# Kernel optimization log

Hardware: AMD Instinct MI355X
Metric: run time of the kernel (lower is better)

The kernel has to match this reference:

```python
import jax, jax.numpy as jnp
import numpy as np

MAX_DEG = 3
DEG_DIMS = [1, 3, 5, 7]          # degree_to_dim(d) = 2d+1
SUM_DIM = 16                     # sum of DEG_DIMS
FREQ_SUM = 44                    # sum over (d_in,d_out) of 2*min(d_in,d_out)+1
C = 32                           # channels per degree (in == out, FULL fusion)
EDGE_DIM = 2                     # fiber_edge[0] + 1
MID = 32                         # RadialProfile mid_dim
E = 4096
N = 1024


def setup_inputs() -> dict:
    key = jax.random.key(0)
    ks = jax.random.split(key, 16)
    inp = {}
    for d, dim in enumerate(DEG_DIMS):
        inp[f"node_feats_{d}"] = jax.random.normal(ks[d], (N, C, dim), jnp.float32)
    inp["edge_feats_0"] = jax.random.normal(ks[4], (E, EDGE_DIM, 1), jnp.float32)
    inp["basis"] = jax.random.normal(ks[5], (E, SUM_DIM, FREQ_SUM, SUM_DIM), jnp.float32)
    inp["src"] = jax.random.randint(ks[6], (E,), 0, N, dtype=jnp.int32)
    inp["dst"] = jax.random.randint(ks[7], (E,), 0, N, dtype=jnp.int32)
    # RadialProfile params: Linear(2,32) -> ReLU -> Linear(32,32) -> ReLU -> Linear(32, 44*32*32, bias=False)
    inp["w1"] = jax.random.normal(ks[8], (EDGE_DIM, MID), jnp.float32) / np.sqrt(EDGE_DIM)
    inp["b1"] = jnp.zeros((MID,), jnp.float32)
    inp["w2"] = jax.random.normal(ks[9], (MID, MID), jnp.float32) / np.sqrt(MID)
    inp["b2"] = jnp.zeros((MID,), jnp.float32)
    inp["w3"] = jax.random.normal(ks[10], (MID, FREQ_SUM * C * C), jnp.float32) / np.sqrt(MID)
    # self-interaction kernels per output degree
    for d in range(MAX_DEG + 1):
        inp[f"kernel_self_{d}"] = jax.random.normal(ks[11 + d], (C, C), jnp.float32) / np.sqrt(C)
    return inp


def _conv_se3(node_feats, edge_feats_0, basis, src, dst,
              w1, b1, w2, b2, w3, kernels_self):
    e = edge_feats_0.shape[0]
    # invariant edge feats: [E, edge_dim]
    inv = edge_feats_0[..., 0]
    # gather source node features and fuse along representation dim: [E, C, 16]
    feats = jnp.concatenate([nf[src] for nf in node_feats], axis=-1)
    # RadialProfile MLP -> radial weights [E, C_out, C_in * FREQ_SUM]
    h = jax.nn.relu(inv @ w1 + b1)
    h = jax.nn.relu(h @ w2 + b2)
    radial_weights = (h @ w3).reshape(e, C, C * FREQ_SUM)
    # VersatileConvSE3 fused path:
    # tmp = (features @ basis_view).view(E, C*FREQ_SUM, SUM_DIM)
    basis_view = basis.reshape(e, SUM_DIM, FREQ_SUM * SUM_DIM)
    tmp = jnp.einsum('eci,eix->ecx', feats, basis_view).reshape(e, C * FREQ_SUM, SUM_DIM)
    out_fused = jnp.einsum('eok,eks->eos', radial_weights, tmp)  # [E, C, 16]
    # unfuse by degree, add self-interaction at dst, pool (copy_e_sum) to nodes
    outs = []
    off = 0
    for d, dim in enumerate(DEG_DIMS):
        o = out_fused[..., off:off + dim]
        o = o + jnp.einsum('oc,ecd->eod', kernels_self[d], node_feats[d][dst])
        outs.append(jax.ops.segment_sum(o, dst, num_segments=N))
        off += dim
    # return fused node output [N, C, 16] (concat of degrees 0..3)
    return jnp.concatenate(outs, axis=-1)


def reference(node_feats_0, node_feats_1, node_feats_2, node_feats_3,
              edge_feats_0, basis, src, dst,
              w1, b1, w2, b2, w3,
              kernel_self_0, kernel_self_1, kernel_self_2, kernel_self_3):
    return _conv_se3([node_feats_0, node_feats_1, node_feats_2, node_feats_3],
                     edge_feats_0, basis, src, dst,
                     w1, b1, w2, b2, w3,
                     [kernel_self_0, kernel_self_1, kernel_self_2, kernel_self_3])
```

## Files before the change

### kernel.cpp

```cpp
#include <hip/hip_runtime.h>
#include <hip/hip_bf16.h>

#define NN 1024
#define EE 4096
#define CC 32
#define SD 16
#define FQ 44
#define MIDC 32
#define EB 16
#define NFQ 4
#define FPB 11

typedef short s16x4 __attribute__((ext_vector_type(4)));
typedef short s16x8 __attribute__((ext_vector_type(8)));
typedef float fx4 __attribute__((ext_vector_type(4)));

__device__ __forceinline__ unsigned short f2b(float x) {
    __hip_bfloat16 b = __float2bfloat16(x);
    return *reinterpret_cast<unsigned short*>(&b);
}

__device__ __forceinline__ s16x4 pack4(float a, float b, float c, float d) {
    s16x4 r;
    r[0] = (short)f2b(a); r[1] = (short)f2b(b);
    r[2] = (short)f2b(c); r[3] = (short)f2b(d);
    return r;
}

__device__ __forceinline__ fx4 mfma16(s16x4 a, s16x4 b, fx4 c) {
#if defined(__HIP_DEVICE_COMPILE__)
#if __has_builtin(__builtin_amdgcn_mfma_f32_16x16x16_bf16)
    return __builtin_amdgcn_mfma_f32_16x16x16_bf16(a, b, c, 0, 0, 0);
#else
    return __builtin_amdgcn_mfma_f32_16x16x16bf16_1k(a, b, c, 0, 0, 0);
#endif
#else
    return c;
#endif
}

#define CBAR() asm volatile("s_waitcnt lgkmcnt(0)\n\ts_barrier" ::: "memory")
#define MEMFENCE() asm volatile("" ::: "memory")

__global__ __launch_bounds__(256) void k_w3t2(const float* __restrict__ w3,
                                              unsigned short* __restrict__ w3t2) {
    int tid = blockIdx.x * 256 + threadIdx.x;
    int m = tid & 31;
    int o = (tid >> 5) & 31;
    int c = tid >> 10;
    const float* rp = &w3[(size_t)m * 45056 + o * 1408 + c * 44];
    float v[44];
#pragma unroll
    for (int q = 0; q < 11; q++) {
        float4 t4 = *(const float4*)(rp + q * 4);
        v[q * 4 + 0] = t4.x; v[q * 4 + 1] = t4.y;
        v[q * 4 + 2] = t4.z; v[q * 4 + 3] = t4.w;
    }
#pragma unroll
    for (int f = 0; f < FQ; f++) {
        w3t2[(((size_t)f * CC + o) * CC + c) * CC + m] = f2b(v[f]);
    }
}

__global__ __launch_bounds__(256) void k_h(const float* __restrict__ ef,
                                           const float* __restrict__ w1,
                                           const float* __restrict__ b1,
                                           const float* __restrict__ w2,
                                           const float* __restrict__ b2,
                                           const int* __restrict__ dst,
                                           unsigned short* __restrict__ h2,
                                           int* __restrict__ deg) {
    int e = blockIdx.x * 256 + threadIdx.x;
    if (e >= EE) return;
    float i0 = ef[e * 2 + 0], i1 = ef[e * 2 + 1];
    float h1[MIDC];
#pragma unroll
    for (int j = 0; j < MIDC; j++) {
        float v = i0 * w1[j] + i1 * w1[MIDC + j] + b1[j];
        h1[j] = v > 0.f ? v : 0.f;
    }
    for (int j = 0; j < MIDC; j++) {
        float v = b2[j];
#pragma unroll
        for (int m = 0; m < MIDC; m++) v += h1[m] * w2[m * MIDC + j];
        v = v > 0.f ? v : 0.f;
        h2[e * MIDC + j] = f2b(v);
    }
    atomicAdd(&deg[dst[e]], 1);
}

__global__ __launch_bounds__(512, 4) void k_main(
    const float* __restrict__ nf0, const float* __restrict__ nf1,
    const float* __restrict__ nf2, const float* __restrict__ nf3,
    const float* __restrict__ basis, const int* __restrict__ src,
    const int* __restrict__ dst, const unsigned short* __restrict__ h2,
    const unsigned short* __restrict__ w3t2, float* __restrict__ out) {
    __shared__ __align__(16) unsigned short rad_lds[EB * CC * CC];

    int t = threadIdx.x;
    int wv = t >> 6;
    int l = t & 63;
    int l15 = l & 15;
    int kg = l >> 4;
    int fq = blockIdx.x >> 8;
    int eg = blockIdx.x & 255;
    int eb = eg * EB;
    int f0 = fq * FPB;

    s16x8 h2frag = *(const s16x8*)(h2 + ((size_t)(eb + l15) * MIDC + (kg << 3)));

    s16x4 fa[2][2];
#pragma unroll
    for (int ei = 0; ei < 2; ei++) {
        int sn = src[eb + (wv << 1) + ei];
#pragma unroll
        for (int ch = 0; ch < 2; ch++) {
            int c = (ch << 4) + l15;
            s16x4 v;
#pragma unroll
            for (int j = 0; j < 4; j++) {
                int i = (kg << 2) + j;
                float x;
                if (i < 1) x = nf0[sn * CC + c];
                else if (i < 4) x = nf1[(sn * CC + c) * 3 + (i - 1)];
                else if (i < 9) x = nf2[(sn * CC + c) * 5 + (i - 4)];
                else x = nf3[(sn * CC + c) * 7 + (i - 9)];
                v[j] = (short)f2b(x);
            }
            fa[ei][ch] = v;
        }
    }

    int radw[8];
#pragma unroll
    for (int j = 0; j < 8; j++) {
        int o = (wv << 2) + (j >> 1), ch = j & 1;
        int b = (l15 << 11) | (o << 6) | (ch << 5) | (kg << 3);
        radw[j] = b ^ (((l15 ^ o) & 15) << 3);
    }
    int rada[2][2][2];
#pragma unroll
    for (int ei = 0; ei < 2; ei++) {
        int e = (wv << 1) + ei;
#pragma unroll
        for (int oh = 0; oh < 2; oh++) {
            int o = (oh << 4) + l15;
#pragma unroll
            for (int ch = 0; ch < 2; ch++) {
                int b = (e << 11) | (o << 6) | (ch << 5) | (kg << 3);
                rada[ei][oh][ch] = b ^ (((e ^ o) & 15) << 3);
            }
        }
    }

    fx4 acc[2][2];
#pragma unroll
    for (int q = 0; q < 4; q++) acc[q >> 1][q & 1] = (fx4){0.f, 0.f, 0.f, 0.f};
    fx4 zz = (fx4){0.f, 0.f, 0.f, 0.f};

    s16x8 w[8];
    float pfA[2][4], pfB[2][4];

#define LOAD_W(F)                                                                       \
    {                                                                                   \
        _Pragma("unroll") for (int j = 0; j < 8; j++) {                                 \
            int o_ = (wv << 2) + (j >> 1), ch_ = j & 1;                                 \
            w[j] = *(const s16x8*)(w3t2 +                                               \
                ((((size_t)(F) * CC + o_) * CC + (ch_ << 4) + l15) * CC + (kg << 3)));  \
        }                                                                               \
        MEMFENCE();                                                                     \
    }
#define LOAD_PF(F, SLOT)                                                                \
    {                                                                                   \
        _Pragma("unroll") for (int ei_ = 0; ei_ < 2; ei_++) {                           \
            const float* bp = basis +                                                   \
                (((size_t)(eb + (wv << 1) + ei_) * SD + (kg << 2)) * FQ + (F)) * SD +   \
                l15;                                                                    \
            _Pragma("unroll") for (int j = 0; j < 4; j++)                               \
                SLOT[ei_][j] = bp[(size_t)j * (FQ * SD)];                               \
        }                                                                               \
        MEMFENCE();                                                                     \
    }

    LOAD_PF(f0, pfA);
    LOAD_W(f0);
    LOAD_PF(f0 + 1, pfB);

#pragma unroll
    for (int fi = 0; fi < FPB; fi++) {
        int f = f0 + fi;
#pragma unroll
        for (int j = 0; j < 8; j++) {
            fx4 cf = __builtin_amdgcn_mfma_f32_16x16x32_bf16(w[j], h2frag, zz, 0, 0, 0);
            *(s16x4*)((char*)rad_lds + radw[j]) = pack4(cf[0], cf[1], cf[2], cf[3]);
        }
        if (fi + 1 < FPB) LOAD_W(f + 1);

        s16x4 bbf[2];
        if ((fi & 1) == 0) {
            bbf[0] = pack4(pfA[0][0], pfA[0][1], pfA[0][2], pfA[0][3]);
            bbf[1] = pack4(pfA[1][0], pfA[1][1], pfA[1][2], pfA[1][3]);
            if (fi + 2 < FPB) { LOAD_PF(f + 2, pfA); }
        } else {
            bbf[0] = pack4(pfB[0][0], pfB[0][1], pfB[0][2], pfB[0][3]);
            bbf[1] = pack4(pfB[1][0], pfB[1][1], pfB[1][2], pfB[1][3]);
            if (fi + 2 < FPB) { LOAD_PF(f + 2, pfB); }
        }
        CBAR();

#pragma unroll
        for (int ei = 0; ei < 2; ei++) {
#pragma unroll
            for (int ch = 0; ch < 2; ch++) {
                fx4 u = mfma16(fa[ei][ch], bbf[ei], zz);
                s16x4 ub = pack4(u[0], u[1], u[2], u[3]);
#pragma unroll
                for (int oh = 0; oh < 2; oh++) {
                    s16x4 ra = *(const s16x4*)((char*)rad_lds + rada[ei][oh][ch]);
                    acc[ei][oh] = mfma16(ra, ub, acc[ei][oh]);
                }
            }
        }
        if (fi + 1 < FPB) CBAR();
    }

#pragma unroll
    for (int ei = 0; ei < 2; ei++) {
        int e = (wv << 1) + ei;
        int d = dst[eb + e];
        float* op = &out[(size_t)d * (CC * SD)];
#pragma unroll
        for (int oh = 0; oh < 2; oh++) {
#pragma unroll
            for (int r = 0; r < 4; r++) {
                int o = (oh << 4) + (kg << 2) + r;
                atomicAdd(&op[o * SD + l15], acc[ei][oh][r]);
            }
        }
    }
}

__global__ __launch_bounds__(256) void k_self(
    const float* __restrict__ nf0, const float* __restrict__ nf1,
    const float* __restrict__ nf2, const float* __restrict__ nf3,
    const float* __restrict__ ks0, const float* __restrict__ ks1,
    const float* __restrict__ ks2, const float* __restrict__ ks3,
    const int* __restrict__ deg, float* __restrict__ out) {
    int idx = blockIdx.x * 256 + threadIdx.x;
    if (idx >= NN * CC * SD) return;
    int n = idx >> 9;
    int rem = idx & 511;
    int o = rem >> 4;
    int s = rem & 15;
    const float* nf;
    const float* ks;
    int dim, off;
    if (s < 1) { nf = nf0; ks = ks0; dim = 1; off = 0; }
    else if (s < 4) { nf = nf1; ks = ks1; dim = 3; off = 1; }
    else if (s < 9) { nf = nf2; ks = ks2; dim = 5; off = 4; }
    else { nf = nf3; ks = ks3; dim = 7; off = 9; }
    int j = s - off;
    float acc = 0.f;
#pragma unroll
    for (int c = 0; c < CC; c++) acc += ks[o * CC + c] * nf[(n * CC + c) * dim + j];
    out[idx] += (float)deg[n] * acc;
}

extern "C" void kernel_launch(void* const* d_in, const int* in_sizes, int n_in,
                              void* d_out, int out_size, void* d_ws, size_t ws_size,
                              hipStream_t stream) {
    const float* nf0 = (const float*)d_in[0];
    const float* nf1 = (const float*)d_in[1];
    const float* nf2 = (const float*)d_in[2];
    const float* nf3 = (const float*)d_in[3];
    const float* ef = (const float*)d_in[4];
    const float* basis = (const float*)d_in[5];
    const int* src = (const int*)d_in[6];
    const int* dst = (const int*)d_in[7];
    const float* w1 = (const float*)d_in[8];
    const float* b1 = (const float*)d_in[9];
    const float* w2 = (const float*)d_in[10];
    const float* b2 = (const float*)d_in[11];
    const float* w3 = (const float*)d_in[12];
    const float* ks0 = (const float*)d_in[13];
    const float* ks1 = (const float*)d_in[14];
    const float* ks2 = (const float*)d_in[15];
    const float* ks3 = (const float*)d_in[16];
    float* out = (float*)d_out;

    unsigned short* h2 = (unsigned short*)d_ws;
    int* deg = (int*)((char*)d_ws + EE * MIDC * 2);
    unsigned short* w3t2 = (unsigned short*)((char*)d_ws + EE * MIDC * 2 + 4096);

    (void)hipMemsetAsync(d_out, 0, (size_t)out_size * sizeof(float), stream);
    (void)hipMemsetAsync(deg, 0, NN * sizeof(int), stream);

    k_w3t2<<<128, 256, 0, stream>>>(w3, w3t2);
    k_h<<<EE / 256, 256, 0, stream>>>(ef, w1, b1, w2, b2, dst, h2, deg);
    k_main<<<(EE / EB) * NFQ, 512, 0, stream>>>(nf0, nf1, nf2, nf3, basis, src, dst,
                                                h2, w3t2, out);
    k_self<<<(NN * CC * SD) / 256, 256, 0, stream>>>(nf0, nf1, nf2, nf3, ks0, ks1,
                                                     ks2, ks3, deg, out);
}
```

Baseline: 126.6 us.

## Stage basis slice into LDS with coalesced float4 loads before frequency loop

```diff
diff --git a/kernel.cpp b/kernel.cpp
--- a/kernel.cpp
+++ b/kernel.cpp
@@ -10,6 +10,8 @@
 #define EB 16
 #define NFQ 4
 #define FPB 11
+#define FSTR 264
+#define ESTR (FPB * FSTR)
 
 typedef short s16x4 __attribute__((ext_vector_type(4)));
 typedef short s16x8 __attribute__((ext_vector_type(8)));
@@ -89,19 +91,19 @@
     atomicAdd(&deg[dst[e]], 1);
 }
 
-__global__ __launch_bounds__(512, 4) void k_main(
+__global__ __launch_bounds__(512, 2) void k_main(
     const float* __restrict__ nf0, const float* __restrict__ nf1,
     const float* __restrict__ nf2, const float* __restrict__ nf3,
     const float* __restrict__ basis, const int* __restrict__ src,
     const int* __restrict__ dst, const unsigned short* __restrict__ h2,
     const unsigned short* __restrict__ w3t2, float* __restrict__ out) {
     __shared__ __align__(16) unsigned short rad_lds[EB * CC * CC];
+    __shared__ __align__(16) unsigned short basT[EB * ESTR];
 
     int t = threadIdx.x;
     int wv = t >> 6;
-    int l = t & 63;
-    int l15 = l & 15;
-    int kg = l >> 4;
+    int l15 = t & 15;
+    int kg = (t >> 4) & 3;
     int fq = blockIdx.x >> 8;
     int eg = blockIdx.x & 255;
     int eb = eg * EB;
@@ -131,6 +133,21 @@
         }
     }
 
+#pragma unroll
+    for (int k = 0; k < 22; k++) {
+        int fi4 = k * 512 + t;
+        int g = fi4 / 44;
+        int r = fi4 - g * 44;
+        int e = g >> 4, i = g & 15;
+        const float4* sp = (const float4*)basis +
+                           (((size_t)(eb + e) * SD + i) * 176 + fq * 44 + r);
+        float4 v = *sp;
+        int perm = ((i & 3) << 2) | (i >> 2);
+        int f1 = r >> 2, s0 = (r & 3) << 2;
+        *(s16x4*)(&basT[e * ESTR + f1 * FSTR + perm * 16 + s0]) =
+            pack4(v.x, v.y, v.z, v.w);
+    }
+
     int radw[8];
 #pragma unroll
     for (int j = 0; j < 8; j++) {
@@ -159,8 +176,6 @@
     fx4 zz = (fx4){0.f, 0.f, 0.f, 0.f};
 
     s16x8 w[8];
-    float pfA[2][4], pfB[2][4];
-
 #define LOAD_W(F)                                                                       \
     {                                                                                   \
         _Pragma("unroll") for (int j = 0; j < 8; j++) {                                 \
@@ -170,44 +185,35 @@
         }                                                                               \
         MEMFENCE();                                                                     \
     }
-#define LOAD_PF(F, SLOT)                                                                \
-    {                                                                                   \
-        _Pragma("unroll") for (int ei_ = 0; ei_ < 2; ei_++) {                           \
-            const float* bp = basis +                                                   \
-                (((size_t)(eb + (wv << 1) + ei_) * SD + (kg << 2)) * FQ + (F)) * SD +   \
-                l15;                                                                    \
-            _Pragma("unroll") for (int j = 0; j < 4; j++)                               \
-                SLOT[ei_][j] = bp[(size_t)j * (FQ * SD)];                               \
-        }                                                                               \
-        MEMFENCE();                                                                     \
-    }
-
-    LOAD_PF(f0, pfA);
+
     LOAD_W(f0);
-    LOAD_PF(f0 + 1, pfB);
+    __syncthreads();
 
 #pragma unroll
     for (int fi = 0; fi < FPB; fi++) {
         int f = f0 + fi;
+        __builtin_amdgcn_s_setprio(1);
 #pragma unroll
         for (int j = 0; j < 8; j++) {
             fx4 cf = __builtin_amdgcn_mfma_f32_16x16x32_bf16(w[j], h2frag, zz, 0, 0, 0);
             *(s16x4*)((char*)rad_lds + radw[j]) = pack4(cf[0], cf[1], cf[2], cf[3]);
         }
+        __builtin_amdgcn_s_setprio(0);
         if (fi + 1 < FPB) LOAD_W(f + 1);
 
         s16x4 bbf[2];
-        if ((fi & 1) == 0) {
-            bbf[0] = pack4(pfA[0][0], pfA[0][1], pfA[0][2], pfA[0][3]);
-            bbf[1] = pack4(pfA[1][0], pfA[1][1], pfA[1][2], pfA[1][3]);
-            if (fi + 2 < FPB) { LOAD_PF(f + 2, pfA); }
-        } else {
-            bbf[0] = pack4(pfB[0][0], pfB[0][1], pfB[0][2], pfB[0][3]);
-            bbf[1] = pack4(pfB[1][0], pfB[1][1], pfB[1][2], pfB[1][3]);
-            if (fi + 2 < FPB) { LOAD_PF(f + 2, pfB); }
+#pragma unroll
+        for (int ei = 0; ei < 2; ei++) {
+            const unsigned short* bp =
+                &basT[((wv << 1) + ei) * ESTR + fi * FSTR + (kg << 4) + l15];
+            s16x4 v;
+#pragma unroll
+            for (int j = 0; j < 4; j++) v[j] = (short)bp[j << 6];
+            bbf[ei] = v;
         }
         CBAR();
 
+        __builtin_amdgcn_s_setprio(1);
 #pragma unroll
         for (int ei = 0; ei < 2; ei++) {
 #pragma unroll
@@ -221,6 +227,7 @@
                 }
             }
         }
+        __builtin_amdgcn_s_setprio(0);
         if (fi + 1 < FPB) CBAR();
     }
 
```

Result: slower. 144.2 us (+13.8%).
